# Kernel tuning notes

Measured on AMD Instinct MI355X. Metric: run time of the kernel, lower is better.

## Reference

```python
import jax, jax.numpy as jnp
import numpy as np

KTOP = 64


def setup_inputs() -> dict:
    key = jax.random.key(0)
    x = jax.random.normal(key, (32, 16384, 128), dtype=jnp.float32)
    return {"x": x}


def reference(x) -> jnp.ndarray:
    # k-max pooling along axis 1, preserving original order.
    # x: [B, L, C] -> out: [B, KTOP, C]
    idx = jnp.argsort(x, axis=1)[:, -KTOP:, :]      # indices of the KTOP largest per (b, c)
    idx = jnp.sort(idx, axis=1)                      # restore original temporal order
    return jnp.take_along_axis(x, idx, axis=1)       # [B, KTOP, C]
```

## Files before the change

### kernel.cpp

```cpp
#include <hip/hip_runtime.h>
#include <math.h>
#include <stdint.h>

#define B_     32
#define L_     16384
#define C_     128
#define KTOP   64
#define NCOL   (B_ * C_)
#define CAPMAX 256
#define CSTR   32
#define LSLOT  16
#define T0     2.42f

typedef float f32x4 __attribute__((ext_vector_type(4)));

__device__ __forceinline__ uint64_t pack_cand(float v, int l) {
    return ((uint64_t)__float_as_uint(v) << 32) | (uint32_t)l;
}

__device__ __forceinline__ bool lex_lt(float v1, int i1, float v2, int i2) {
    return (v1 < v2) || ((v1 == v2) && (i1 < i2));
}

__global__ __launch_bounds__(256) void k_zero(int* __restrict__ cnt) {
    cnt[blockIdx.x * 256 + threadIdx.x] = 0;
}

__global__ __launch_bounds__(256) void k_filter(const float* __restrict__ x,
                                                int* __restrict__ cnt,
                                                uint64_t* __restrict__ cand,
                                                int cap) {
    __shared__ int      lcnt[C_];
    __shared__ uint64_t lbuf[C_][LSLOT + 1];

    const int tid = threadIdx.x;
    const int b   = blockIdx.y;
    const int l0  = blockIdx.x * 256;
    const int r   = tid >> 5;
    const int c4  = tid & 31;
    const f32x4* xb = (const f32x4*)x + (size_t)b * L_ * (C_ / 4);
    const int clbase = c4 * 4;

    if (tid < C_) lcnt[tid] = 0;
    __syncthreads();

    for (int l = l0 + r; l < l0 + 256; l += 16) {
        f32x4 v0 = xb[(size_t)l * (C_ / 4) + c4];
        f32x4 v1 = xb[(size_t)(l + 8) * (C_ / 4) + c4];
#pragma unroll
        for (int h = 0; h < 2; ++h) {
            const f32x4 v = h ? v1 : v0;
            const int   lr = l + h * 8;
#pragma unroll
            for (int j = 0; j < 4; ++j) {
                float vv = (j == 0) ? v.x : (j == 1) ? v.y : (j == 2) ? v.z : v.w;
                if (vv > T0) {
                    int cl = clbase + j;
                    int p  = atomicAdd(&lcnt[cl], 1);
                    if (p < LSLOT) {
                        lbuf[cl][p] = pack_cand(vv, lr);
                    } else {
                        int g = atomicAdd(&cnt[(b * C_ + cl) * CSTR], 1);
                        if (g < cap) cand[(size_t)(b * C_ + cl) * cap + g] = pack_cand(vv, lr);
                    }
                }
            }
        }
    }
    __syncthreads();

    if (tid < C_) {
        int m = lcnt[tid];
        m = (m > LSLOT) ? LSLOT : m;
        if (m > 0) {
            int col  = b * C_ + tid;
            int base = atomicAdd(&cnt[col * CSTR], m);
            for (int j = 0; j < m; ++j) {
                int p = base + j;
                if (p < cap) cand[(size_t)col * cap + p] = lbuf[tid][j];
            }
        }
    }
}

__global__ __launch_bounds__(256) void k_select(const float* __restrict__ x,
                                                const int* __restrict__ cnt,
                                                const uint64_t* __restrict__ cand,
                                                float* __restrict__ out,
                                                int cap) {
    const int wave = threadIdx.x >> 6;
    const int lane = threadIdx.x & 63;
    const int col  = blockIdx.x * 4 + wave;
    const int b    = col >> 7;
    const int c    = col & (C_ - 1);

    const int n = (cap > 0) ? cnt[col * CSTR] : 0;

    float keepv = 0.0f;
    int   keepi = 0;

    if (n >= KTOP && n <= cap) {
        uint64_t s[4];
#pragma unroll
        for (int i = 0; i < 4; ++i) {
            int p = lane + i * 64;
            s[i] = (p < n) ? cand[(size_t)col * cap + p] : 0ull;
        }
#pragma unroll
        for (int k = 2; k <= 256; k <<= 1) {
#pragma unroll
            for (int j = k >> 1; j >= 64; j >>= 1) {
                const int rd = j >> 6;
#pragma unroll
                for (int r = 0; r < 4; ++r) {
                    if ((r & rd) == 0) {
                        const int q = r | rd;
                        const bool km = (((r * 64) & k) == 0);
                        uint64_t hi = (s[r] > s[q]) ? s[r] : s[q];
                        uint64_t lo = (s[r] > s[q]) ? s[q] : s[r];
                        s[r] = km ? hi : lo;
                        s[q] = km ? lo : hi;
                    }
                }
            }
#pragma unroll
            for (int j = (k >> 1) > 32 ? 32 : (k >> 1); j >= 1; j >>= 1) {
                const bool upper = (lane & j) != 0;
#pragma unroll
                for (int r = 0; r < 4; ++r) {
                    uint64_t o = __shfl_xor((unsigned long long)s[r], j, 64);
                    const bool km = (((r * 64 + lane) & k) == 0);
                    const bool take_max = (km != upper);
                    const bool gt = s[r] > o;
                    s[r] = (take_max == gt) ? s[r] : o;
                }
            }
        }
        keepv = __uint_as_float((uint32_t)(s[0] >> 32));
        keepi = (int)(uint32_t)(s[0] & 0xffffffffull);
    } else {
        const float* xc = x + (size_t)b * L_ * C_ + c;
        float pv = INFINITY;
        int   pi = 0x7fffffff;
        for (int k = 0; k < KTOP; ++k) {
            float bv = -INFINITY;
            int   bi = -1;
            for (int l = lane; l < L_; l += 64) {
                float vv = xc[(size_t)l * C_];
                if (lex_lt(vv, l, pv, pi) && lex_lt(bv, bi, vv, l)) {
                    bv = vv; bi = l;
                }
            }
#pragma unroll
            for (int off = 32; off; off >>= 1) {
                float ov = __shfl_xor(bv, off, 64);
                int   oi = __shfl_xor(bi, off, 64);
                if (lex_lt(bv, bi, ov, oi)) { bv = ov; bi = oi; }
            }
            pv = bv; pi = bi;
            if (lane == k) { keepv = bv; keepi = bi; }
        }
    }

    uint64_t key2 = ((uint64_t)(uint32_t)keepi << 32) | __float_as_uint(keepv);
#pragma unroll
    for (int k = 2; k <= 64; k <<= 1) {
#pragma unroll
        for (int j = k >> 1; j >= 1; j >>= 1) {
            const bool upper = (lane & j) != 0;
            uint64_t o = __shfl_xor((unsigned long long)key2, j, 64);
            const bool km = ((lane & k) != 0);
            const bool take_max = (km != upper);
            const bool gt = key2 > o;
            key2 = (take_max == gt) ? key2 : o;
        }
    }
    out[((size_t)b * KTOP + lane) * C_ + c] =
        __uint_as_float((uint32_t)(key2 & 0xffffffffull));
}

extern "C" void kernel_launch(void* const* d_in, const int* in_sizes, int n_in,
                              void* d_out, int out_size, void* d_ws, size_t ws_size,
                              hipStream_t stream) {
    (void)in_sizes; (void)n_in; (void)out_size;
    const float* x  = (const float*)d_in[0];
    float*      out = (float*)d_out;

    int*   cnt       = (int*)d_ws;
    size_t cnt_bytes = (size_t)NCOL * CSTR * sizeof(int);

    int cap = 0;
    if (ws_size > cnt_bytes) {
        size_t rem = ws_size - cnt_bytes;
        size_t c   = rem / ((size_t)NCOL * 8);
        cap = (c > CAPMAX) ? CAPMAX : (int)c;
    }
    uint64_t* cand = (uint64_t*)((char*)d_ws + cnt_bytes);

    if (cap >= KTOP) {
        k_zero<<<(NCOL * CSTR) / 256, 256, 0, stream>>>(cnt);
        dim3 g1(L_ / 256, B_);
        k_filter<<<g1, 256, 0, stream>>>(x, cnt, cand, cap);
    } else {
        cap = 0;
    }

    k_select<<<NCOL / 4, 256, 0, stream>>>(x, cnt, cand, out, cap);
}
```

Before: 70.84 us.

## Replace 256-wide bitonic sort with ballot-based radix threshold search in select

The candidate top-64 selection stops using a full 256-element bitonic sort over 64-bit keys and instead binary-searches the value threshold with wave ballots and popcounts. A second binary search over indices breaks ties, and winners are compacted into LDS by prefix popcount before the existing index-order sort. This removes many 64-bit shuffles and compares per column. The cost is about 30 serial ballot iterations of the value search, plus correctness that depends on positive float bit patterns above T0 ordering correctly as unsigned integers.

```diff
diff --git a/kernel.cpp b/kernel.cpp
--- a/kernel.cpp
+++ b/kernel.cpp
@@ -88,6 +88,8 @@
                                                 const uint64_t* __restrict__ cand,
                                                 float* __restrict__ out,
                                                 int cap) {
+    __shared__ uint64_t wbuf[4][KTOP];
+
     const int wave = threadIdx.x >> 6;
     const int lane = threadIdx.x & 63;
     const int col  = blockIdx.x * 4 + wave;
@@ -96,52 +98,65 @@
 
     const int n = (cap > 0) ? cnt[col * CSTR] : 0;
 
-    float keepv = 0.0f;
-    int   keepi = 0;
+    uint64_t key2;
 
     if (n >= KTOP && n <= cap) {
-        uint64_t s[4];
+        uint32_t vb[4], ix[4];
 #pragma unroll
         for (int i = 0; i < 4; ++i) {
             int p = lane + i * 64;
-            s[i] = (p < n) ? cand[(size_t)col * cap + p] : 0ull;
-        }
-#pragma unroll
-        for (int k = 2; k <= 256; k <<= 1) {
-#pragma unroll
-            for (int j = k >> 1; j >= 64; j >>= 1) {
-                const int rd = j >> 6;
-#pragma unroll
-                for (int r = 0; r < 4; ++r) {
-                    if ((r & rd) == 0) {
-                        const int q = r | rd;
-                        const bool km = (((r * 64) & k) == 0);
-                        uint64_t hi = (s[r] > s[q]) ? s[r] : s[q];
-                        uint64_t lo = (s[r] > s[q]) ? s[q] : s[r];
-                        s[r] = km ? hi : lo;
-                        s[q] = km ? lo : hi;
-                    }
-                }
-            }
-#pragma unroll
-            for (int j = (k >> 1) > 32 ? 32 : (k >> 1); j >= 1; j >>= 1) {
-                const bool upper = (lane & j) != 0;
-#pragma unroll
-                for (int r = 0; r < 4; ++r) {
-                    uint64_t o = __shfl_xor((unsigned long long)s[r], j, 64);
-                    const bool km = (((r * 64 + lane) & k) == 0);
-                    const bool take_max = (km != upper);
-                    const bool gt = s[r] > o;
-                    s[r] = (take_max == gt) ? s[r] : o;
-                }
-            }
-        }
-        keepv = __uint_as_float((uint32_t)(s[0] >> 32));
-        keepi = (int)(uint32_t)(s[0] & 0xffffffffull);
+            uint64_t s = (p < n) ? cand[(size_t)col * cap + p] : 0ull;
+            vb[i] = (uint32_t)(s >> 32);
+            ix[i] = (uint32_t)s;
+        }
+        uint32_t vmax = max(max(vb[0], vb[1]), max(vb[2], vb[3]));
+#pragma unroll
+        for (int off = 32; off; off >>= 1)
+            vmax = max(vmax, (uint32_t)__shfl_xor((int)vmax, off, 64));
+        uint32_t lo = __float_as_uint(T0), hi = vmax + 1;
+        while (hi - lo > 1) {
+            uint32_t mid = lo + ((hi - lo) >> 1);
+            int cgt = 0;
+#pragma unroll
+            for (int i = 0; i < 4; ++i)
+                cgt += (int)__popcll(__ballot(vb[i] > mid));
+            if (cgt >= KTOP) lo = mid; else hi = mid;
+        }
+        const uint32_t v64 = lo + 1;
+        int cgt = 0;
+#pragma unroll
+        for (int i = 0; i < 4; ++i)
+            cgt += (int)__popcll(__ballot(vb[i] > v64));
+        const int m = KTOP - cgt;
+        uint32_t tlo = 0, thi = L_;
+        while (thi - tlo > 1) {
+            uint32_t mid = tlo + ((thi - tlo) >> 1);
+            int ct = 0;
+#pragma unroll
+            for (int i = 0; i < 4; ++i)
+                ct += (int)__popcll(__ballot(vb[i] == v64 && ix[i] >= mid));
+            if (ct >= m) tlo = mid; else thi = mid;
+        }
+        volatile uint64_t* wb = wbuf[wave];
+        int base = 0;
+#pragma unroll
+        for (int i = 0; i < 4; ++i) {
+            const bool win = (vb[i] > v64) || (vb[i] == v64 && ix[i] >= tlo);
+            const uint64_t msk = __ballot(win);
+            if (win) {
+                int slot = base + (int)__popcll(msk & ((1ull << lane) - 1ull));
+                wb[slot] = ((uint64_t)ix[i] << 32) | vb[i];
+            }
+            base += (int)__popcll(msk);
+        }
+        __builtin_amdgcn_wave_barrier();
+        key2 = wb[lane];
     } else {
         const float* xc = x + (size_t)b * L_ * C_ + c;
         float pv = INFINITY;
         int   pi = 0x7fffffff;
+        float keepv = 0.0f;
+        int   keepi = 0;
         for (int k = 0; k < KTOP; ++k) {
             float bv = -INFINITY;
             int   bi = -1;
@@ -160,9 +175,9 @@
             pv = bv; pi = bi;
             if (lane == k) { keepv = bv; keepi = bi; }
         }
-    }
-
-    uint64_t key2 = ((uint64_t)(uint32_t)keepi << 32) | __float_as_uint(keepv);
+        key2 = ((uint64_t)(uint32_t)keepi << 32) | __float_as_uint(keepv);
+    }
+
 #pragma unroll
     for (int k = 2; k <= 64; k <<= 1) {
 #pragma unroll
```

Measured after the change: 66.47 us. 6.2% less time.
